# Kernel optimization log

Measured on AMD Instinct MI355X. Metric: run time of the kernel, lower is better.

## Reference

```python
import jax, jax.numpy as jnp
import numpy as np

BS, SEQ, D, H = 2, 2048, 1024, 16
HD = D // H  # head_dim = 64


def setup_inputs() -> dict:
    key = jax.random.key(0)
    kx, kw = jax.random.split(key)
    x = jax.random.normal(kx, (BS, SEQ, D), dtype=jnp.float32)
    # qkv Linear: weight [3D, D] (xavier_normal), bias zeros
    std = float(np.sqrt(2.0 / (D + 3 * D)))
    W_qkv = jax.random.normal(kw, (3 * D, D), dtype=jnp.float32) * std
    b_qkv = jnp.zeros((3 * D,), dtype=jnp.float32)
    return {"x": x, "W_qkv": W_qkv, "b_qkv": b_qkv}


def reference(x, W_qkv, b_qkv):
    bs, seq_len, embed_dim = x.shape
    # fused QKV projection: [bs, seq, 3D]
    qkv = x @ W_qkv.T + b_qkv
    qkv = qkv.reshape(bs, seq_len, 3, H, HD)
    qkv = jnp.transpose(qkv, (2, 0, 3, 1, 4))  # [3, bs, H, seq, HD]
    Q, K, V = qkv[0], qkv[1], qkv[2]
    # past_kv is None -> total_len == seq_len, past_len == 0
    scores = jnp.einsum("bhqd,bhkd->bhqk", Q, K) / jnp.sqrt(jnp.float32(HD))
    # causal mask: True above diagonal -> -inf
    mask = jnp.triu(jnp.ones((seq_len, seq_len), dtype=bool), k=1)
    scores = jnp.where(mask[None, None, :, :], -jnp.inf, scores)
    probs = jax.nn.softmax(scores, axis=-1)
    # attn_dropout = 0.0 (eval) -> identity
    out = jnp.einsum("bhqk,bhkd->bhqd", probs, V)
    out = jnp.transpose(out, (0, 2, 1, 3)).reshape(bs, seq_len, embed_dim)
    return (out, (K, V))
```

## Files before the change

kernel.cpp:

```cpp
#include <hip/hip_runtime.h>

typedef __bf16 bf16_t;
typedef __bf16 bf16x8 __attribute__((ext_vector_type(8)));
typedef float f32x4 __attribute__((ext_vector_type(4)));

__device__ __forceinline__ unsigned short bfbits(float f) {
  unsigned u = __float_as_uint(f);
  u += 0x7fffu + ((u >> 16) & 1u);
  return (unsigned short)(u >> 16);
}
__device__ __forceinline__ bf16_t f2bf(float f) {
  unsigned short s = bfbits(f);
  union { unsigned short s; bf16_t b; } cv; cv.s = s; return cv.b;
}

__device__ __forceinline__ void gl16(const void* g, void* l) {
  __builtin_amdgcn_global_load_lds(
      (const __attribute__((address_space(1))) void*)g,
      (__attribute__((address_space(3))) void*)l,
      16, 0, 0);
}

__global__ __launch_bounds__(256) void cvt_kernel(const float* __restrict__ x,
                                                  const float* __restrict__ Wf,
                                                  bf16_t* __restrict__ xb,
                                                  bf16_t* __restrict__ wb) {
  const int i = blockIdx.x * 256 + threadIdx.x;
  const float* src; bf16_t* dst; int j;
  if (i < 524288) { j = i; src = x; dst = xb; }
  else            { j = i - 524288; src = Wf; dst = wb; }
  const float4* s = (const float4*)src + (size_t)j * 2;
  float4 a = s[0], b = s[1];
  bf16x8 o;
  o[0] = f2bf(a.x); o[1] = f2bf(a.y); o[2] = f2bf(a.z); o[3] = f2bf(a.w);
  o[4] = f2bf(b.x); o[5] = f2bf(b.y); o[6] = f2bf(b.z); o[7] = f2bf(b.w);
  const int row = j >> 7, jr = j & 127;
  const int dstc = (row << 7) + (jr & ~3) + ((jr & 3) ^ ((row >> 1) & 3));
  *((bf16x8*)dst + dstc) = o;
}

#define GEMM_K 1024
__global__ __launch_bounds__(256) void qkv_gemm(
    const bf16_t* __restrict__ A,
    const bf16_t* __restrict__ B,
    const float* __restrict__ bias,
    float* __restrict__ Ko, float* __restrict__ Vo,
    bf16_t* __restrict__ Qb, bf16_t* __restrict__ Kb,
    bf16_t* __restrict__ Vt,
    int* __restrict__ qcnt)
{
  if (blockIdx.x == 0 && threadIdx.x == 0) *qcnt = 0;
  __shared__ bf16_t lsA[128 * 32];
  __shared__ bf16_t lsB[128 * 32];
  const int tid = threadIdx.x;
  const int lane = tid & 63;
  const int ln = lane & 15, qd = lane >> 4;
  const int wid = tid >> 6;
  const int wm = wid & 1, wn = wid >> 1;
  const int bm = blockIdx.x & 31, bn = blockIdx.x >> 5;
  const int m0 = bm * 128, n0 = bn * 128;
  const int qs = qd ^ ((ln >> 1) & 3);

  f32x4 acc[4][4] = {};

  const int c0 = tid, c1 = tid + 256;
  const bf16_t* ga0 = A + (size_t)(m0 + (c0 >> 2)) * GEMM_K + (c0 & 3) * 8;
  const bf16_t* ga1 = A + (size_t)(m0 + (c1 >> 2)) * GEMM_K + (c1 & 3) * 8;
  const bf16_t* gb0 = B + (size_t)(n0 + (c0 >> 2)) * GEMM_K + (c0 & 3) * 8;
  const bf16_t* gb1 = B + (size_t)(n0 + (c1 >> 2)) * GEMM_K + (c1 & 3) * 8;
  bf16_t* la0 = &lsA[c0 * 8];
  bf16_t* la1 = &lsA[c1 * 8];
  bf16_t* lb0 = &lsB[c0 * 8];
  bf16_t* lb1 = &lsB[c1 * 8];

  for (int k0 = 0; k0 < GEMM_K; k0 += 32) {
    __syncthreads();
    gl16(ga0 + k0, la0);
    gl16(ga1 + k0, la1);
    gl16(gb0 + k0, lb0);
    gl16(gb1 + k0, lb1);
    __syncthreads();
    bf16x8 af[4], bf[4];
#pragma unroll
    for (int mi = 0; mi < 4; ++mi)
      af[mi] = *(const bf16x8*)&lsA[(wm * 64 + mi * 16 + ln) * 32 + qs * 8];
#pragma unroll
    for (int ni = 0; ni < 4; ++ni)
      bf[ni] = *(const bf16x8*)&lsB[(wn * 64 + ni * 16 + ln) * 32 + qs * 8];
#pragma unroll
    for (int mi = 0; mi < 4; ++mi)
#pragma unroll
      for (int ni = 0; ni < 4; ++ni)
        acc[mi][ni] = __builtin_amdgcn_mfma_f32_16x16x32_bf16(af[mi], bf[ni], acc[mi][ni], 0, 0, 0);
  }

  const int sec = n0 >> 10;
#pragma unroll
  for (int mi = 0; mi < 4; ++mi) {
#pragma unroll
    for (int ni = 0; ni < 4; ++ni) {
      const int colg = n0 + wn * 64 + ni * 16 + ln;
      const float bv = bias[colg];
      const int cc = colg & 1023, h = cc >> 6, hd = cc & 63;
#pragma unroll
      for (int r = 0; r < 4; ++r) {
        const int mg = m0 + wm * 64 + mi * 16 + qd * 4 + r;
        const int b = mg >> 11, s = mg & 2047;
        const float val = acc[mi][ni][r] + bv;
        const int bhi = b * 16 + h;
        const size_t pidx = ((size_t)(bhi * 2048 + s)) * 64 + hd;
        const size_t sidx = (size_t)bhi * 131072 + (size_t)(s >> 6) * 4096 +
                            (size_t)(s & 63) * 64 + (((hd >> 3) ^ (s & 7)) << 3) + (hd & 7);
        if (sec == 0) {
          Qb[sidx] = f2bf(val);
        } else if (sec == 1) {
          Ko[pidx] = val;
          Kb[sidx] = f2bf(val);
        } else {
          Vo[pidx] = val;
          const size_t vidx = (size_t)bhi * 131072 + (size_t)(s >> 6) * 4096 +
                              (size_t)hd * 64 + ((((s >> 3) & 7) ^ (hd & 7)) << 3) + (s & 7);
          Vt[vidx] = f2bf(val);
        }
      }
    }
  }
}

__global__ __launch_bounds__(256) void attn_kernel(
    const bf16_t* __restrict__ Qb,
    const bf16_t* __restrict__ Kb,
    const bf16_t* __restrict__ Vt,
    float* __restrict__ Out,
    int* __restrict__ qcnt)
{
  __shared__ bf16_t lq[128 * 64];
  __shared__ bf16_t lk[2][64 * 64];
  __shared__ bf16_t lv[2][64 * 64];
  __shared__ bf16_t lp[128 * 64];
  __shared__ int task_sh;
  const int tid = threadIdx.x;
  const int lane = tid & 63, ln = lane & 15, qd = lane >> 4;
  const int w = tid >> 6;
  const int l7 = ln & 7;
  const float C1 = 0.125f * 1.44269504f;

  for (;;) {
    __syncthreads();
    if (tid == 0) task_sh = atomicAdd(qcnt, 1);
    __syncthreads();
    const int task = task_sh;
    if (task >= 512) break;
    const int it = 15 - (task >> 5);
    const int bh = task & 31;
    const int b = bh >> 4, h = bh & 15;
    const int jt1 = 2 * it + 2;

    const bf16_t* qbase = Qb + (size_t)bh * 131072 + (size_t)it * 8192;
    const bf16_t* kbase = Kb + (size_t)bh * 131072;
    const bf16_t* vbase = Vt + (size_t)bh * 131072;

#pragma unroll
    for (int i = 0; i < 4; ++i) { const int cc = tid + i * 256; gl16(qbase + cc * 8, &lq[cc * 8]); }
    {
      const int cc = tid, c2 = tid + 256;
      gl16(kbase + cc * 8, &lk[0][cc * 8]);
      gl16(kbase + c2 * 8, &lk[0][c2 * 8]);
      gl16(vbase + cc * 8, &lv[0][cc * 8]);
      gl16(vbase + c2 * 8, &lv[0][c2 * 8]);
    }
    __syncthreads();

    bf16x8 afq[2][2];
#pragma unroll
    for (int kk = 0; kk < 2; ++kk)
#pragma unroll
      for (int qi = 0; qi < 2; ++qi) {
        const int row = w * 32 + qi * 16 + ln;
        afq[kk][qi] = *(const bf16x8*)&lq[(row >> 6) * 4096 + (row & 63) * 64 +
                                          (((kk * 4 + qd) ^ l7) << 3)];
      }

    f32x4 oc[2][4] = {};
    float lsum[2] = {0.f, 0.f};
    const int qg = it * 128 + w * 32 + ln;

    for (int jt = 0; jt < jt1; ++jt) {
      if (jt > 0) __syncthreads();
      const int cur = jt & 1;
      if (jt + 1 < jt1) {
        const bf16_t* kt = kbase + (size_t)(jt + 1) * 4096;
        const bf16_t* vt = vbase + (size_t)(jt + 1) * 4096;
        const int nxt = cur ^ 1;
        const int cc = tid, c2 = tid + 256;
        gl16(kt + cc * 8, &lk[nxt][cc * 8]);
        gl16(kt + c2 * 8, &lk[nxt][c2 * 8]);
        gl16(vt + cc * 8, &lv[nxt][cc * 8]);
        gl16(vt + c2 * 8, &lv[nxt][c2 * 8]);
      }

      f32x4 sa[4][2] = {};
#pragma unroll
      for (int kk = 0; kk < 2; ++kk) {
        bf16x8 ak[4];
#pragma unroll
        for (int ki = 0; ki < 4; ++ki)
          ak[ki] = *(const bf16x8*)&lk[cur][(ki * 16 + ln) * 64 + (((kk * 4 + qd) ^ l7) << 3)];
#pragma unroll
        for (int ki = 0; ki < 4; ++ki)
#pragma unroll
          for (int qi = 0; qi < 2; ++qi)
            sa[ki][qi] = __builtin_amdgcn_mfma_f32_16x16x32_bf16(ak[ki], afq[kk][qi], sa[ki][qi], 0, 0, 0);
      }

      const bool diag = (jt >= 2 * it);
#pragma unroll
      for (int qi = 0; qi < 2; ++qi) {
        const int qgl = qg + qi * 16;
        const int q = w * 32 + qi * 16 + ln;
#pragma unroll
        for (int ki = 0; ki < 4; ++ki) {
          const int kb0 = jt * 64 + ki * 16 + qd * 4;
          unsigned long long pk = 0;
#pragma unroll
          for (int r = 0; r < 4; ++r) {
            float sv = sa[ki][qi][r] * C1;
            if (diag && (kb0 + r > qgl)) sv = -10000.f;
            const float p = __builtin_amdgcn_exp2f(sv);
            lsum[qi] += p;
            pk |= ((unsigned long long)bfbits(p)) << (16 * r);
          }
          const int g = (ki * 2 + (qd >> 1)) ^ l7;
          *(unsigned long long*)&lp[q * 64 + g * 8 + (qd & 1) * 4] = pk;
        }
      }

#pragma unroll
      for (int kk = 0; kk < 2; ++kk) {
        bf16x8 afp[2], bfv[4];
#pragma unroll
        for (int qi = 0; qi < 2; ++qi) {
          const int q = w * 32 + qi * 16 + ln;
          afp[qi] = *(const bf16x8*)&lp[q * 64 + (((kk * 4 + qd) ^ l7) << 3)];
        }
#pragma unroll
        for (int ni = 0; ni < 4; ++ni)
          bfv[ni] = *(const bf16x8*)&lv[cur][(ni * 16 + ln) * 64 + (((kk * 4 + qd) ^ l7) << 3)];
#pragma unroll
        for (int qi = 0; qi < 2; ++qi)
#pragma unroll
          for (int ni = 0; ni < 4; ++ni)
            oc[qi][ni] = __builtin_amdgcn_mfma_f32_16x16x32_bf16(afp[qi], bfv[ni], oc[qi][ni], 0, 0, 0);
      }
    }

    float lsq[2];
#pragma unroll
    for (int qi = 0; qi < 2; ++qi) {
      float ls = lsum[qi];
      ls += __shfl_xor(ls, 16);
      ls += __shfl_xor(ls, 32);
      lsq[qi] = ls;
    }
#pragma unroll
    for (int qi = 0; qi < 2; ++qi) {
#pragma unroll
      for (int r = 0; r < 4; ++r) {
        const float lval = __shfl(lsq[qi], qd * 4 + r);
        const float inv = 1.0f / lval;
        const int rowq = it * 128 + w * 32 + qi * 16 + qd * 4 + r;
#pragma unroll
        for (int ni = 0; ni < 4; ++ni) {
          const int colh = ni * 16 + ln;
          Out[(size_t)(b * 2048 + rowq) * 1024 + h * 64 + colh] = oc[qi][ni][r] * inv;
        }
      }
    }
  }
}

extern "C" void kernel_launch(void* const* d_in, const int* in_sizes, int n_in,
                              void* d_out, int out_size, void* d_ws, size_t ws_size,
                              hipStream_t stream) {
  const float* x = (const float*)d_in[0];
  const float* W = (const float*)d_in[1];
  const float* bq = (const float*)d_in[2];
  float* out = (float*)d_out;
  float* Ko = out + 4194304;
  float* Vo = out + 8388608;
  char* ws = (char*)d_ws;
  bf16_t* xb = (bf16_t*)ws;
  bf16_t* wb = (bf16_t*)(ws + 8388608);
  bf16_t* Qb = (bf16_t*)(ws + 14680064);
  bf16_t* Kb = (bf16_t*)(ws + 23068672);
  bf16_t* Vt = (bf16_t*)(ws + 31457280);
  int*    qcnt = (int*)(ws + 39845888);

  hipLaunchKernelGGL(cvt_kernel, dim3(3584), dim3(256), 0, stream, x, W, xb, wb);
  hipLaunchKernelGGL(qkv_gemm, dim3(768), dim3(256), 0, stream, xb, wb, bq, Ko, Vo, Qb, Kb, Vt, qcnt);
  hipLaunchKernelGGL(attn_kernel, dim3(256), dim3(256), 0, stream, Qb, Kb, Vt, out, qcnt);
}
```

Before: 192.0 us.

## Restructure attention into 128-key stages and run two blocks per CU

After: 182.0 us. 5.2% less time.

```diff
diff --git a/kernel.cpp b/kernel.cpp
--- a/kernel.cpp
+++ b/kernel.cpp
@@ -3,6 +3,7 @@
 typedef __bf16 bf16_t;
 typedef __bf16 bf16x8 __attribute__((ext_vector_type(8)));
 typedef float f32x4 __attribute__((ext_vector_type(4)));
+typedef unsigned long long u64;
 
 __device__ __forceinline__ unsigned short bfbits(float f) {
   unsigned u = __float_as_uint(f);
@@ -112,7 +113,7 @@
         const size_t sidx = (size_t)bhi * 131072 + (size_t)(s >> 6) * 4096 +
                             (size_t)(s & 63) * 64 + (((hd >> 3) ^ (s & 7)) << 3) + (hd & 7);
         if (sec == 0) {
-          Qb[sidx] = f2bf(val);
+          Qb[sidx] = f2bf(val * 0.18033688f);
         } else if (sec == 1) {
           Ko[pidx] = val;
           Kb[sidx] = f2bf(val);
@@ -134,16 +135,15 @@
     float* __restrict__ Out,
     int* __restrict__ qcnt)
 {
-  __shared__ bf16_t lq[128 * 64];
-  __shared__ bf16_t lk[2][64 * 64];
-  __shared__ bf16_t lv[2][64 * 64];
-  __shared__ bf16_t lp[128 * 64];
+  __shared__ bf16_t lq[8192];
+  __shared__ bf16_t lk[8192];
+  __shared__ bf16_t lv[8192];
+  __shared__ bf16_t lp[8192];
   __shared__ int task_sh;
   const int tid = threadIdx.x;
   const int lane = tid & 63, ln = lane & 15, qd = lane >> 4;
   const int w = tid >> 6;
   const int l7 = ln & 7;
-  const float C1 = 0.125f * 1.44269504f;
 
   for (;;) {
     __syncthreads();
@@ -151,23 +151,20 @@
     __syncthreads();
     const int task = task_sh;
     if (task >= 512) break;
-    const int it = 15 - (task >> 5);
+    const int it = (task < 256) ? (15 - (task >> 5)) : ((task - 256) >> 5);
     const int bh = task & 31;
     const int b = bh >> 4, h = bh & 15;
-    const int jt1 = 2 * it + 2;
 
     const bf16_t* qbase = Qb + (size_t)bh * 131072 + (size_t)it * 8192;
     const bf16_t* kbase = Kb + (size_t)bh * 131072;
     const bf16_t* vbase = Vt + (size_t)bh * 131072;
 
 #pragma unroll
-    for (int i = 0; i < 4; ++i) { const int cc = tid + i * 256; gl16(qbase + cc * 8, &lq[cc * 8]); }
-    {
-      const int cc = tid, c2 = tid + 256;
-      gl16(kbase + cc * 8, &lk[0][cc * 8]);
-      gl16(kbase + c2 * 8, &lk[0][c2 * 8]);
-      gl16(vbase + cc * 8, &lv[0][cc * 8]);
-      gl16(vbase + c2 * 8, &lv[0][c2 * 8]);
+    for (int i = 0; i < 4; ++i) {
+      const int cc = tid + i * 256;
+      gl16(qbase + cc * 8, &lq[cc * 8]);
+      gl16(kbase + cc * 8, &lk[cc * 8]);
+      gl16(vbase + cc * 8, &lv[cc * 8]);
     }
     __syncthreads();
 
@@ -185,72 +182,78 @@
     float lsum[2] = {0.f, 0.f};
     const int qg = it * 128 + w * 32 + ln;
 
-    for (int jt = 0; jt < jt1; ++jt) {
-      if (jt > 0) __syncthreads();
-      const int cur = jt & 1;
-      if (jt + 1 < jt1) {
-        const bf16_t* kt = kbase + (size_t)(jt + 1) * 4096;
-        const bf16_t* vt = vbase + (size_t)(jt + 1) * 4096;
-        const int nxt = cur ^ 1;
-        const int cc = tid, c2 = tid + 256;
-        gl16(kt + cc * 8, &lk[nxt][cc * 8]);
-        gl16(kt + c2 * 8, &lk[nxt][c2 * 8]);
-        gl16(vt + cc * 8, &lv[nxt][cc * 8]);
-        gl16(vt + c2 * 8, &lv[nxt][c2 * 8]);
-      }
-
-      f32x4 sa[4][2] = {};
-#pragma unroll
-      for (int kk = 0; kk < 2; ++kk) {
-        bf16x8 ak[4];
-#pragma unroll
-        for (int ki = 0; ki < 4; ++ki)
-          ak[ki] = *(const bf16x8*)&lk[cur][(ki * 16 + ln) * 64 + (((kk * 4 + qd) ^ l7) << 3)];
-#pragma unroll
-        for (int ki = 0; ki < 4; ++ki)
+    for (int st = 0; st <= it; ++st) {
+      if (st > 0) {
+        __syncthreads();
+#pragma unroll
+        for (int i = 0; i < 4; ++i) {
+          const int cc = tid + i * 256;
+          gl16(kbase + (size_t)st * 8192 + cc * 8, &lk[cc * 8]);
+          gl16(vbase + (size_t)st * 8192 + cc * 8, &lv[cc * 8]);
+        }
+        __syncthreads();
+      }
+      const bool diag = (st == it);
+
+#pragma unroll
+      for (int h2 = 0; h2 < 2; ++h2) {
+        const int lofs = h2 * 4096;
+        f32x4 sa[4][2] = {};
+#pragma unroll
+        for (int kk = 0; kk < 2; ++kk) {
+          bf16x8 ak[4];
+#pragma unroll
+          for (int ki = 0; ki < 4; ++ki)
+            ak[ki] = *(const bf16x8*)&lk[lofs + (ki * 16 + ln) * 64 + (((kk * 4 + qd) ^ l7) << 3)];
+#pragma unroll
+          for (int ki = 0; ki < 4; ++ki)
+#pragma unroll
+            for (int qi = 0; qi < 2; ++qi)
+              sa[ki][qi] = __builtin_amdgcn_mfma_f32_16x16x32_bf16(ak[ki], afq[kk][qi], sa[ki][qi], 0, 0, 0);
+        }
+
+#pragma unroll
+        for (int qi = 0; qi < 2; ++qi) {
+          const int qgl = qg + qi * 16;
+          const int q = w * 32 + qi * 16 + ln;
+#pragma unroll
+          for (int ki = 0; ki < 4; ++ki) {
+            const int kb0 = (st * 2 + h2) * 64 + ki * 16 + qd * 4;
+            float p0 = __builtin_amdgcn_exp2f(sa[ki][qi][0]);
+            float p1 = __builtin_amdgcn_exp2f(sa[ki][qi][1]);
+            float p2 = __builtin_amdgcn_exp2f(sa[ki][qi][2]);
+            float p3 = __builtin_amdgcn_exp2f(sa[ki][qi][3]);
+            if (diag) {
+              if (kb0 + 0 > qgl) p0 = 0.f;
+              if (kb0 + 1 > qgl) p1 = 0.f;
+              if (kb0 + 2 > qgl) p2 = 0.f;
+              if (kb0 + 3 > qgl) p3 = 0.f;
+            }
+            lsum[qi] += (p0 + p1) + (p2 + p3);
+            const unsigned lo = (__float_as_uint(p1) & 0xFFFF0000u) | (__float_as_uint(p0) >> 16);
+            const unsigned hi = (__float_as_uint(p3) & 0xFFFF0000u) | (__float_as_uint(p2) >> 16);
+            const int g = (ki * 2 + (qd >> 1)) ^ l7;
+            *(u64*)&lp[q * 64 + g * 8 + (qd & 1) * 4] = ((u64)hi << 32) | lo;
+          }
+        }
+
+#pragma unroll
+        for (int kk = 0; kk < 2; ++kk) {
+          bf16x8 afp[2], bfv[4];
+#pragma unroll
+          for (int qi = 0; qi < 2; ++qi) {
+            const int q = w * 32 + qi * 16 + ln;
+            afp[qi] = *(const bf16x8*)&lp[q * 64 + (((kk * 4 + qd) ^ l7) << 3)];
+          }
+#pragma unroll
+          for (int ni = 0; ni < 4; ++ni)
+            bfv[ni] = *(const bf16x8*)&lv[lofs + (ni * 16 + ln) * 64 + (((kk * 4 + qd) ^ l7) << 3)];
 #pragma unroll
           for (int qi = 0; qi < 2; ++qi)
-            sa[ki][qi] = __builtin_amdgcn_mfma_f32_16x16x32_bf16(ak[ki], afq[kk][qi], sa[ki][qi], 0, 0, 0);
-      }
-
-      const bool diag = (jt >= 2 * it);
-#pragma unroll
-      for (int qi = 0; qi < 2; ++qi) {
-        const int qgl = qg + qi * 16;
-        const int q = w * 32 + qi * 16 + ln;
-#pragma unroll
-        for (int ki = 0; ki < 4; ++ki) {
-          const int kb0 = jt * 64 + ki * 16 + qd * 4;
-          unsigned long long pk = 0;
-#pragma unroll
-          for (int r = 0; r < 4; ++r) {
-            float sv = sa[ki][qi][r] * C1;
-            if (diag && (kb0 + r > qgl)) sv = -10000.f;
-            const float p = __builtin_amdgcn_exp2f(sv);
-            lsum[qi] += p;
-            pk |= ((unsigned long long)bfbits(p)) << (16 * r);
-          }
-          const int g = (ki * 2 + (qd >> 1)) ^ l7;
-          *(unsigned long long*)&lp[q * 64 + g * 8 + (qd & 1) * 4] = pk;
-        }
-      }
-
-#pragma unroll
-      for (int kk = 0; kk < 2; ++kk) {
-        bf16x8 afp[2], bfv[4];
-#pragma unroll
-        for (int qi = 0; qi < 2; ++qi) {
-          const int q = w * 32 + qi * 16 + ln;
-          afp[qi] = *(const bf16x8*)&lp[q * 64 + (((kk * 4 + qd) ^ l7) << 3)];
-        }
-#pragma unroll
-        for (int ni = 0; ni < 4; ++ni)
-          bfv[ni] = *(const bf16x8*)&lv[cur][(ni * 16 + ln) * 64 + (((kk * 4 + qd) ^ l7) << 3)];
-#pragma unroll
-        for (int qi = 0; qi < 2; ++qi)
-#pragma unroll
-          for (int ni = 0; ni < 4; ++ni)
-            oc[qi][ni] = __builtin_amdgcn_mfma_f32_16x16x32_bf16(afp[qi], bfv[ni], oc[qi][ni], 0, 0, 0);
+#pragma unroll
+            for (int ni = 0; ni < 4; ++ni)
+              oc[qi][ni] = __builtin_amdgcn_mfma_f32_16x16x32_bf16(afp[qi], bfv[ni], oc[qi][ni], 0, 0, 0);
+        }
       }
     }
 
@@ -298,5 +301,5 @@
 
   hipLaunchKernelGGL(cvt_kernel, dim3(3584), dim3(256), 0, stream, x, W, xb, wb);
   hipLaunchKernelGGL(qkv_gemm, dim3(768), dim3(256), 0, stream, xb, wb, bq, Ko, Vo, Qb, Kb, Vt, qcnt);
-  hipLaunchKernelGGL(attn_kernel, dim3(256), dim3(256), 0, stream, Qb, Kb, Vt, out, qcnt);
-}
+  hipLaunchKernelGGL(attn_kernel, dim3(512), dim3(256), 0, stream, Qb, Kb, Vt, out, qcnt);
+}
```
